# Performance work log

Measured on AMD Instinct MI355X. Metric: run time of the kernel, lower is better.

The kernel has to match this reference:

```python
import jax, jax.numpy as jnp
import numpy as np

N_USERS = 100000
N_ITEMS = 50000
DIM = 64
HID = 64
E = 3200000
B = 16384


def setup_inputs() -> dict:
    key = jax.random.key(0)
    ks = jax.random.split(key, 16)
    N = N_USERS + N_ITEMS
    return {
        "users": jax.random.randint(ks[0], (B,), 0, N_USERS),
        "items": jax.random.randint(ks[1], (B,), 0, N_ITEMS),
        "edge_index": jax.random.randint(ks[2], (2, E), 0, N),
        "edge_weight": jax.random.uniform(ks[3], (E,), dtype=jnp.float32),
        # learned parameters
        "U": jax.random.normal(ks[4], (N_USERS, DIM), jnp.float32) * 0.1,
        "I": jax.random.normal(ks[5], (N_ITEMS, DIM), jnp.float32) * 0.1,
        "W0": jax.random.normal(ks[6], (DIM, HID), jnp.float32) / np.sqrt(DIM),
        "b0": jnp.zeros((HID,), jnp.float32),
        "g0": jnp.ones((HID,), jnp.float32),
        "be0": jnp.zeros((HID,), jnp.float32),
        "W1": jax.random.normal(ks[7], (HID, HID), jnp.float32) / np.sqrt(HID),
        "b1": jnp.zeros((HID,), jnp.float32),
        "g1": jnp.ones((HID,), jnp.float32),
        "be1": jnp.zeros((HID,), jnp.float32),
        "Wp": jax.random.normal(ks[8], (HID, DIM), jnp.float32) / np.sqrt(HID),
        "bp": jnp.zeros((DIM,), jnp.float32),
        "bu": jnp.zeros((N_USERS,), jnp.float32),
        "bi": jnp.zeros((N_ITEMS,), jnp.float32),
        "mu": jnp.zeros((), jnp.float32),
    }


def _layernorm(h, g, b, eps=1e-5):
    m = jnp.mean(h, axis=-1, keepdims=True)
    v = jnp.mean(jnp.square(h - m), axis=-1, keepdims=True)
    return (h - m) * jax.lax.rsqrt(v + eps) * g + b


def reference(users, items, edge_index, edge_weight, U, I,
              W0, b0, g0, be0, W1, b1, g1, be1, Wp, bp, bu, bi, mu):
    N = U.shape[0] + I.shape[0]
    x = jnp.concatenate([U, I], axis=0)  # [N, DIM]

    # GCN normalization with added self-loops (torch_geometric gcn_norm)
    loop = jnp.arange(N)
    src = jnp.concatenate([edge_index[0], loop])
    dst = jnp.concatenate([edge_index[1], loop])
    ew = jnp.concatenate([edge_weight, jnp.ones((N,), edge_weight.dtype)])
    deg = jax.ops.segment_sum(ew, dst, num_segments=N)
    dinv = jnp.where(deg > 0, jax.lax.rsqrt(deg), 0.0)
    norm = dinv[src] * ew * dinv[dst]  # [E+N]

    def conv(h, W, b):
        hw = h @ W  # [N, HID]
        msgs = norm[:, None] * hw[src]  # gather: [E+N, HID]
        return jax.ops.segment_sum(msgs, dst, num_segments=N) + b

    # layer 0: conv -> layernorm -> relu -> (dropout=identity, eval) -> residual
    h = x
    h_in = h
    h = conv(h, W0, b0)
    h = jax.nn.relu(_layernorm(h, g0, be0)) + h_in
    # layer 1
    h_in = h
    h = conv(h, W1, b1)
    h = jax.nn.relu(_layernorm(h, g1, be1)) + h_in

    h = h @ Wp + bp  # proj_out: [N, DIM]
    h_user = h[:U.shape[0]]
    h_item = h[U.shape[0]:]

    s = jnp.sum(h_user[users] * h_item[items], axis=-1)
    s = s + bu[users] + bi[items] + mu
    return jnp.clip(s, 1.0, 5.0)
```

## Files before the change

kernel.cpp:

```cpp
#include <hip/hip_runtime.h>

#define NU 100000
#define NI 50000
#define NN 150000
#define D  64
#define CAP 47
#define OVF_MAX 4096

#define BINSHIFT 8
#define BINW 256
#define NBINS 586
#define BINCAP 5848
#define STAGE_CAP 12
#define EPT 4
#define SPILL_CAP 262144

typedef unsigned int uint;
typedef unsigned short ushort;

__device__ __forceinline__ float half_reduce_add(float v) {
    #pragma unroll
    for (int m = 16; m >= 1; m >>= 1) v += __shfl_xor(v, m, 64);
    return v;
}
__device__ __forceinline__ ushort f2bf(float f) {
    union { float f; uint i; } c; c.f = f;
    uint r = c.i + 0x7FFF + ((c.i >> 16) & 1);
    return (ushort)(r >> 16);
}
__device__ __forceinline__ float lane_bcast(float v, int l) {
    return __int_as_float(__builtin_amdgcn_readlane(__float_as_int(v), l));
}
__device__ __forceinline__ uint enc14(float w) {
    uint b = __float_as_uint(w) + 0x00020000u;
    return b & 0xFFFC0000u;
}
__device__ __forceinline__ float dec14(uint r) {
    return __uint_as_float(r & 0xFFFC0000u);
}
__device__ __forceinline__ void spill_one(int d, uint s, float w,
        uint2* __restrict__ spill, int* __restrict__ spillcnt) {
    int si = atomicAdd(spillcnt, 1);
    if (si < SPILL_CAP) spill[si] = make_uint2(s | enc14(w), (uint)d);
}

__global__ __launch_bounds__(256) void k_bin(
        const int* __restrict__ src, const int* __restrict__ dst,
        const float* __restrict__ ew, int* __restrict__ bincur,
        uint2* __restrict__ binbuf, uint2* __restrict__ spill,
        int* __restrict__ spillcnt, int E) {
    __shared__ uint2 stage[NBINS][STAGE_CAP];
    __shared__ int scnt[NBINS];
    int t = threadIdx.x;
    for (int i = t; i < NBINS; i += 256) scnt[i] = 0;
    __syncthreads();
    const int batch = 256 * EPT;
    for (int base = blockIdx.x * batch; base < E; base += gridDim.x * batch) {
        int dd[EPT]; uint ss[EPT]; float ww[EPT]; int ok[EPT];
        #pragma unroll
        for (int k = 0; k < EPT; ++k) {
            int e = base + k * 256 + t;
            ok[k] = (e < E);
            if (ok[k]) { dd[k] = dst[e]; ss[k] = (uint)src[e]; ww[k] = ew[e]; }
        }
        #pragma unroll
        for (int k = 0; k < EPT; ++k) {
            if (!ok[k]) continue;
            int bin = dd[k] >> BINSHIFT;
            int slot = atomicAdd(&scnt[bin], 1);
            if (slot < STAGE_CAP) {
                stage[bin][slot] = make_uint2(
                    ss[k] | ((uint)(dd[k] & (BINW - 1)) << 18),
                    (uint)__float_as_int(ww[k]));
            } else {
                spill_one(dd[k], ss[k], ww[k], spill, spillcnt);
            }
        }
        __syncthreads();
        for (int bin = t; bin < NBINS; bin += 256) {
            int c = scnt[bin]; if (c > STAGE_CAP) c = STAGE_CAP;
            while (c >= 8) {
                int b0 = atomicAdd(&bincur[bin], 8);
                if (b0 + 8 <= BINCAP) {
                    uint4* o4 = (uint4*)(binbuf + (size_t)bin * BINCAP + b0);
                    uint2* s2 = &stage[bin][c - 8];
                    o4[0] = make_uint4(s2[0].x, s2[0].y, s2[1].x, s2[1].y);
                    o4[1] = make_uint4(s2[2].x, s2[2].y, s2[3].x, s2[3].y);
                    o4[2] = make_uint4(s2[4].x, s2[4].y, s2[5].x, s2[5].y);
                    o4[3] = make_uint4(s2[6].x, s2[6].y, s2[7].x, s2[7].y);
                } else {
                    for (int j = 0; j < 8; ++j) {
                        uint2 r = stage[bin][c - 8 + j];
                        spill_one((bin << BINSHIFT) + (int)(r.x >> 18),
                                  r.x & 0x3FFFFu, __int_as_float((int)r.y),
                                  spill, spillcnt);
                    }
                }
                c -= 8;
            }
            scnt[bin] = c;
        }
        __syncthreads();
    }
    for (int bin = t; bin < NBINS; bin += 256) {
        int c = scnt[bin]; if (c > STAGE_CAP) c = STAGE_CAP;
        if (c > 0) {
            int b0 = atomicAdd(&bincur[bin], c);
            for (int j = 0; j < c; ++j) {
                uint2 r = stage[bin][j];
                if (b0 + j < BINCAP) binbuf[(size_t)bin * BINCAP + b0 + j] = r;
                else spill_one((bin << BINSHIFT) + (int)(r.x >> 18),
                               r.x & 0x3FFFFu, __int_as_float((int)r.y),
                               spill, spillcnt);
            }
        }
    }
}

__global__ __launch_bounds__(256) void k_regroup(
        const int* __restrict__ bincur, const uint2* __restrict__ binbuf,
        const uint2* __restrict__ spill, const int* __restrict__ spillcnt,
        uint* __restrict__ recs, int* __restrict__ cursor,
        float* __restrict__ dinv, int4* __restrict__ ovf,
        int* __restrict__ ovfcnt) {
    __shared__ uint image[256 * CAP];
    __shared__ int cnt[256];
    __shared__ float ovfw[256];
    int t = threadIdx.x;
    int bin = blockIdx.x;
    cnt[t] = 0; ovfw[t] = 0.0f;
    __syncthreads();
    int dbase = bin << BINSHIFT;
    int nrec = bincur[bin]; if (nrec > BINCAP) nrec = BINCAP;
    const uint2* bb = binbuf + (size_t)bin * BINCAP;
    for (int i = t; i < nrec; i += 256) {
        uint2 r = bb[i];
        int dl = (int)(r.x >> 18);
        int slot = atomicAdd(&cnt[dl], 1);
        uint s = r.x & 0x3FFFFu;
        float w = __int_as_float((int)r.y);
        if (slot < CAP) image[dl * CAP + slot] = enc14(w) | s;
        else {
            atomicAdd(&ovfw[dl], w);
            int o = atomicAdd(ovfcnt, 1);
            if (o < OVF_MAX)
                ovf[o] = make_int4(dbase + dl, (int)s, __float_as_int(w), 0);
        }
    }
    int ns = spillcnt[0]; if (ns > SPILL_CAP) ns = SPILL_CAP;
    for (int i = t; i < ns; i += 256) {
        uint2 e = spill[i];
        int d = (int)e.y;
        if (d < dbase || d >= dbase + BINW) continue;
        int dl = d - dbase;
        int slot = atomicAdd(&cnt[dl], 1);
        if (slot < CAP) image[dl * CAP + slot] = e.x;
        else {
            float w = dec14(e.x);
            atomicAdd(&ovfw[dl], w);
            int o = atomicAdd(ovfcnt, 1);
            if (o < OVF_MAX) ovf[o] = make_int4(d, (int)(e.x & 0x3FFFFu),
                                                __float_as_int(w), 0);
        }
    }
    __syncthreads();
    int ndl = NN - dbase; if (ndl > 256) ndl = 256;
    if (ndl <= 0) return;
    if (t < ndl) {
        int c = cnt[t];
        cursor[dbase + t] = c;
        if (c > CAP) c = CAP;
        float dg = ovfw[t];
        for (int j = 0; j < c; ++j) dg += dec14(image[t * CAP + j]);
        dinv[dbase + t] = rsqrtf(dg + 1.0f);
    }
    int tot = ndl * CAP;
    uint* out = recs + (size_t)dbase * CAP;
    for (int i = t; i < tot; i += 256) out[i] = image[i];
}

__global__ __launch_bounds__(256) void k_gemm(
        const float* __restrict__ h, const float* __restrict__ U,
        const float* __restrict__ I, const float* __restrict__ W,
        const float* __restrict__ dinv, ushort* __restrict__ out) {
    int lane = threadIdx.x & 63;
    float wreg[64];
    #pragma unroll
    for (int k = 0; k < 64; ++k) wreg[k] = W[k * 64 + lane];
    int wpb = blockDim.x >> 6;
    int wid = blockIdx.x * wpb + (threadIdx.x >> 6);
    int tw = gridDim.x * wpb;
    for (int n = wid; n < NN; n += tw) {
        float xv;
        if (h) xv = h[(size_t)n * D + lane];
        else   xv = (n < NU) ? U[(size_t)n * D + lane]
                             : I[(size_t)(n - NU) * D + lane];
        float acc = 0.f;
        #pragma unroll
        for (int k = 0; k < 64; ++k)
            acc = fmaf(lane_bcast(xv, k), wreg[k], acc);
        out[(size_t)n * D + lane] = f2bf(acc * dinv[n]);
    }
}

__device__ __forceinline__ float2 conv_accum2(int n, int lane,
        const uint* __restrict__ hw2p, const int* __restrict__ cursor,
        const uint* __restrict__ recs, const int4* __restrict__ ovf,
        const int* __restrict__ ovfcnt) {
    int cnt = __builtin_amdgcn_readfirstlane(cursor[n]);
    if (cnt > CAP) cnt = CAP;
    uint rv = (lane < cnt) ? recs[(size_t)n * CAP + lane] : 0u;
    int odd = lane >> 5;
    int laneoff = lane & 31;
    float ax = 0.f, ay = 0.f;
    int cp = (cnt + 7) & ~7;
    for (int j0 = 0; j0 < cp; j0 += 8) {
        #pragma unroll
        for (int k = 0; k < 4; ++k) {
            uint re = (uint)__builtin_amdgcn_readlane((int)rv, j0 + 2 * k);
            uint ro = (uint)__builtin_amdgcn_readlane((int)rv, j0 + 2 * k + 1);
            uint r  = odd ? ro : re;
            int   s = (int)(r & 0x3FFFFu);
            float w = dec14(r);
            uint x = hw2p[(size_t)s * 32 + laneoff];
            ax = fmaf(w, __int_as_float((int)(x << 16)), ax);
            ay = fmaf(w, __int_as_float((int)(x & 0xFFFF0000u)), ay);
        }
    }
    ax += __shfl_xor(ax, 32, 64);
    ay += __shfl_xor(ay, 32, 64);
    uint xs = hw2p[(size_t)n * 32 + laneoff];
    ax += __int_as_float((int)(xs << 16));
    ay += __int_as_float((int)(xs & 0xFFFF0000u));
    int novf = __builtin_amdgcn_readfirstlane(ovfcnt[0]);
    if (novf > 0) {
        if (novf > OVF_MAX) novf = OVF_MAX;
        for (int j = 0; j < novf; ++j) {
            int4 e = ovf[j];
            if (e.x == n) {
                float w = __int_as_float(e.z);
                uint x = hw2p[(size_t)e.y * 32 + laneoff];
                ax = fmaf(w, __int_as_float((int)(x << 16)), ax);
                ay = fmaf(w, __int_as_float((int)(x & 0xFFFF0000u)), ay);
            }
        }
    }
    return make_float2(ax, ay);
}

__device__ __forceinline__ float2 ln_relu2(float2 a, float di, int p,
        const float* __restrict__ b, const float* __restrict__ g,
        const float* __restrict__ be) {
    float2 bb = ((const float2*)b)[p];
    float v0 = fmaf(a.x, di, bb.x);
    float v1 = fmaf(a.y, di, bb.y);
    float m = half_reduce_add(v0 + v1) * (1.0f / 64.0f);
    float d0 = v0 - m, d1 = v1 - m;
    float var = half_reduce_add(d0 * d0 + d1 * d1) * (1.0f / 64.0f);
    float rs = rsqrtf(var + 1e-5f);
    float2 gg = ((const float2*)g)[p];
    float2 ee = ((const float2*)be)[p];
    return make_float2(fmaxf(fmaf(d0 * rs, gg.x, ee.x), 0.0f),
                       fmaxf(fmaf(d1 * rs, gg.y, ee.y), 0.0f));
}

__global__ __launch_bounds__(256) void k_conv1(
        const uint* __restrict__ hw2p, const int* __restrict__ cursor,
        const uint* __restrict__ recs, const int4* __restrict__ ovf,
        const int* __restrict__ ovfcnt, const float* __restrict__ dinv,
        const float* __restrict__ b, const float* __restrict__ g,
        const float* __restrict__ be, const float* __restrict__ U,
        const float* __restrict__ I, float* __restrict__ out) {
    int lane = threadIdx.x & 63;
    int n = __builtin_amdgcn_readfirstlane(blockIdx.x * 4 + (threadIdx.x >> 6));
    if (n >= NN) return;
    float2 a = conv_accum2(n, lane, hw2p, cursor, recs, ovf, ovfcnt);
    int p = lane & 31;
    float2 y = ln_relu2(a, dinv[n], p, b, g, be);
    const float* R = (n < NU) ? (U + (size_t)n * D) : (I + (size_t)(n - NU) * D);
    float2 rr = ((const float2*)R)[p];
    if (lane < 32)
        ((float2*)out)[(size_t)n * 32 + p] = make_float2(y.x + rr.x, y.y + rr.y);
}

__global__ __launch_bounds__(256) void k_conv2score(
        const uint* __restrict__ hw2p, const int* __restrict__ cursor,
        const uint* __restrict__ recs, const int4* __restrict__ ovf,
        const int* __restrict__ ovfcnt, const float* __restrict__ dinv,
        const float* __restrict__ b, const float* __restrict__ g,
        const float* __restrict__ be, const int* __restrict__ users,
        const int* __restrict__ items, const float* __restrict__ h1,
        const float* __restrict__ Wp, const float* __restrict__ bp,
        const float* __restrict__ bu, const float* __restrict__ bi,
        const float* __restrict__ mu, float* __restrict__ out, int B) {
    int lane = threadIdx.x & 63;
    float wreg[64];
    #pragma unroll
    for (int k = 0; k < 64; ++k) wreg[k] = Wp[k * 64 + lane];
    float bpl = bp[lane];
    int q = lane & 31;
    int wpb = blockDim.x >> 6;
    int wid = blockIdx.x * wpb + (threadIdx.x >> 6);
    int tw = gridDim.x * wpb;
    for (int p = wid; p < B; p += tw) {
        int un = users[p];
        int in = NU + items[p];
        int nu = __builtin_amdgcn_readfirstlane(un);
        float2 au = conv_accum2(nu, lane, hw2p, cursor, recs, ovf, ovfcnt);
        float2 yu = ln_relu2(au, dinv[nu], q, b, g, be);
        float2 ru = ((const float2*)h1)[(size_t)nu * 32 + q];
        float2 hu = make_float2(yu.x + ru.x, yu.y + ru.y);
        int ni = __builtin_amdgcn_readfirstlane(in);
        float2 ai = conv_accum2(ni, lane, hw2p, cursor, recs, ovf, ovfcnt);
        float2 yi = ln_relu2(ai, dinv[ni], q, b, g, be);
        float2 ri = ((const float2*)h1)[(size_t)ni * 32 + q];
        float2 hi = make_float2(yi.x + ri.x, yi.y + ri.y);
        float pu = bpl, pi = bpl;
        #pragma unroll
        for (int j = 0; j < 32; ++j) {
            pu = fmaf(lane_bcast(hu.x, j), wreg[2 * j], pu);
            pu = fmaf(lane_bcast(hu.y, j), wreg[2 * j + 1], pu);
            pi = fmaf(lane_bcast(hi.x, j), wreg[2 * j], pi);
            pi = fmaf(lane_bcast(hi.y, j), wreg[2 * j + 1], pi);
        }
        float t = pu * pi;
        #pragma unroll
        for (int m = 32; m >= 1; m >>= 1) t += __shfl_xor(t, m, 64);
        if (lane == 0) {
            t += bu[un] + bi[in - NU] + mu[0];
            out[p] = fminf(fmaxf(t, 1.0f), 5.0f);
        }
    }
}

extern "C" void kernel_launch(void* const* d_in, const int* in_sizes, int n_in,
                              void* d_out, int out_size, void* d_ws, size_t ws_size,
                              hipStream_t stream) {
    const int*   users = (const int*)d_in[0];
    const int*   items = (const int*)d_in[1];
    const int*   ei2   = (const int*)d_in[2];
    const float* ew    = (const float*)d_in[3];
    const float* U     = (const float*)d_in[4];
    const float* I     = (const float*)d_in[5];
    const float* W0    = (const float*)d_in[6];
    const float* b0    = (const float*)d_in[7];
    const float* g0    = (const float*)d_in[8];
    const float* be0   = (const float*)d_in[9];
    const float* W1    = (const float*)d_in[10];
    const float* b1    = (const float*)d_in[11];
    const float* g1    = (const float*)d_in[12];
    const float* be1   = (const float*)d_in[13];
    const float* Wp    = (const float*)d_in[14];
    const float* bp    = (const float*)d_in[15];
    const float* bu    = (const float*)d_in[16];
    const float* bi    = (const float*)d_in[17];
    const float* mu    = (const float*)d_in[18];

    int B = in_sizes[0];
    int E = in_sizes[2] / 2;
    const int* srcp = ei2;
    const int* dstp = ei2 + E;

    char* p = (char*)d_ws;
    auto alloc = [&](size_t bytes) -> char* {
        char* r = p;
        p += (bytes + 255) & ~(size_t)255;
        return r;
    };
    int*    cbuf    = (int*)  alloc((size_t)(NBINS + 8) * 4);
    int*    bincur  = cbuf;
    int*    spillcnt= cbuf + NBINS;
    int*    ovfcnt  = cbuf + NBINS + 1;
    int*    cursor  = (int*)  alloc((size_t)NN * 4);
    float*  dinv    = (float*)alloc((size_t)NN * 4);
    int4*   ovf     = (int4*) alloc((size_t)OVF_MAX * 16);
    uint2*  spill   = (uint2*)alloc((size_t)SPILL_CAP * 8);
    uint2*  binbuf  = (uint2*)alloc((size_t)NBINS * BINCAP * 8);
    uint*   recs    = (uint*) alloc((size_t)NN * CAP * 4);
    ushort* hw2b    = (ushort*)alloc((size_t)NN * D * 2);
    float*  h1      = (float*)alloc((size_t)NN * D * 4);
    const uint* hw2p = (const uint*)hw2b;

    hipMemsetAsync(cbuf, 0, (size_t)(NBINS + 8) * 4, stream);

    int gW = (NN + 3) / 4;

    k_bin<<<768, 256, 0, stream>>>(srcp, dstp, ew, bincur, binbuf,
                                   spill, spillcnt, E);
    k_regroup<<<NBINS, 256, 0, stream>>>(bincur, binbuf, spill, spillcnt,
                                         recs, cursor, dinv, ovf, ovfcnt);

    k_gemm<<<2048, 256, 0, stream>>>(nullptr, U, I, W0, dinv, hw2b);
    k_conv1<<<gW, 256, 0, stream>>>(hw2p, cursor, recs, ovf, ovfcnt, dinv,
                                    b0, g0, be0, U, I, h1);
    k_gemm<<<2048, 256, 0, stream>>>(h1, U, I, W1, dinv, hw2b);
    k_conv2score<<<1024, 256, 0, stream>>>(hw2p, cursor, recs, ovf, ovfcnt, dinv,
                                           b1, g1, be1, users, items, h1,
                                           Wp, bp, bu, bi, mu,
                                           (float*)d_out, B);
}
```

Measured before the change: 413.5 us.

## Fuse first GEMM into binning kernel, store h1 in bf16, pipeline conv gathers

The first GEMM now runs inside the binning launch on extra blocks so both overlap, and the dinv scaling is applied afterwards in the regroup kernel on the bf16 output. The layer-1 output h1 is stored as bf16 instead of fp32, which halves its write and read traffic in the second GEMM and the scoring kernel, at some cost in accuracy. The conv gather loop is rewritten as a software-pipelined, manually unrolled sequence using ds_bpermute with three register groups, so more gathers are in flight at once. The GEMM inner loops use four accumulators. Taken together these add rounding steps and register pressure.

```diff
diff --git a/kernel.cpp b/kernel.cpp
--- a/kernel.cpp
+++ b/kernel.cpp
@@ -14,6 +14,8 @@
 #define STAGE_CAP 12
 #define EPT 4
 #define SPILL_CAP 262144
+#define BIN_BLOCKS 768
+#define GEMM_BLOCKS 2048
 
 typedef unsigned int uint;
 typedef unsigned short ushort;
@@ -44,18 +46,42 @@
     if (si < SPILL_CAP) spill[si] = make_uint2(s | enc14(w), (uint)d);
 }
 
-__global__ __launch_bounds__(256) void k_bin(
+__global__ __launch_bounds__(256) void k_bin_gemm(
         const int* __restrict__ src, const int* __restrict__ dst,
         const float* __restrict__ ew, int* __restrict__ bincur,
         uint2* __restrict__ binbuf, uint2* __restrict__ spill,
-        int* __restrict__ spillcnt, int E) {
+        int* __restrict__ spillcnt, int E,
+        const float* __restrict__ U, const float* __restrict__ I,
+        const float* __restrict__ W0, ushort* __restrict__ hw2b) {
     __shared__ uint2 stage[NBINS][STAGE_CAP];
     __shared__ int scnt[NBINS];
+    if (blockIdx.x >= BIN_BLOCKS) {
+        int lane = threadIdx.x & 63;
+        float wreg[64];
+        #pragma unroll
+        for (int k = 0; k < 64; ++k) wreg[k] = W0[k * 64 + lane];
+        int wid = (blockIdx.x - BIN_BLOCKS) * 4 + (threadIdx.x >> 6);
+        int tw = GEMM_BLOCKS * 4;
+        for (int n = wid; n < NN; n += tw) {
+            float xv = (n < NU) ? U[(size_t)n * D + lane]
+                                : I[(size_t)(n - NU) * D + lane];
+            float a0 = 0.f, a1 = 0.f, a2 = 0.f, a3 = 0.f;
+            #pragma unroll
+            for (int k = 0; k < 64; k += 4) {
+                a0 = fmaf(lane_bcast(xv, k + 0), wreg[k + 0], a0);
+                a1 = fmaf(lane_bcast(xv, k + 1), wreg[k + 1], a1);
+                a2 = fmaf(lane_bcast(xv, k + 2), wreg[k + 2], a2);
+                a3 = fmaf(lane_bcast(xv, k + 3), wreg[k + 3], a3);
+            }
+            hw2b[(size_t)n * D + lane] = f2bf((a0 + a1) + (a2 + a3));
+        }
+        return;
+    }
     int t = threadIdx.x;
     for (int i = t; i < NBINS; i += 256) scnt[i] = 0;
     __syncthreads();
     const int batch = 256 * EPT;
-    for (int base = blockIdx.x * batch; base < E; base += gridDim.x * batch) {
+    for (int base = blockIdx.x * batch; base < E; base += BIN_BLOCKS * batch) {
         int dd[EPT]; uint ss[EPT]; float ww[EPT]; int ok[EPT];
         #pragma unroll
         for (int k = 0; k < EPT; ++k) {
@@ -122,7 +148,7 @@
         const uint2* __restrict__ spill, const int* __restrict__ spillcnt,
         uint* __restrict__ recs, int* __restrict__ cursor,
         float* __restrict__ dinv, int4* __restrict__ ovf,
-        int* __restrict__ ovfcnt) {
+        int* __restrict__ ovfcnt, ushort* __restrict__ hw2b) {
     __shared__ uint image[256 * CAP];
     __shared__ int cnt[256];
     __shared__ float ovfw[256];
@@ -172,34 +198,22 @@
         if (c > CAP) c = CAP;
         float dg = ovfw[t];
         for (int j = 0; j < c; ++j) dg += dec14(image[t * CAP + j]);
-        dinv[dbase + t] = rsqrtf(dg + 1.0f);
+        float dv = rsqrtf(dg + 1.0f);
+        dinv[dbase + t] = dv;
+        ovfw[t] = dv;
     }
     int tot = ndl * CAP;
     uint* out = recs + (size_t)dbase * CAP;
     for (int i = t; i < tot; i += 256) out[i] = image[i];
-}
-
-__global__ __launch_bounds__(256) void k_gemm(
-        const float* __restrict__ h, const float* __restrict__ U,
-        const float* __restrict__ I, const float* __restrict__ W,
-        const float* __restrict__ dinv, ushort* __restrict__ out) {
-    int lane = threadIdx.x & 63;
-    float wreg[64];
-    #pragma unroll
-    for (int k = 0; k < 64; ++k) wreg[k] = W[k * 64 + lane];
-    int wpb = blockDim.x >> 6;
-    int wid = blockIdx.x * wpb + (threadIdx.x >> 6);
-    int tw = gridDim.x * wpb;
-    for (int n = wid; n < NN; n += tw) {
-        float xv;
-        if (h) xv = h[(size_t)n * D + lane];
-        else   xv = (n < NU) ? U[(size_t)n * D + lane]
-                             : I[(size_t)(n - NU) * D + lane];
-        float acc = 0.f;
-        #pragma unroll
-        for (int k = 0; k < 64; ++k)
-            acc = fmaf(lane_bcast(xv, k), wreg[k], acc);
-        out[(size_t)n * D + lane] = f2bf(acc * dinv[n]);
+    __syncthreads();
+    uint* hw = (uint*)hw2b + (size_t)dbase * 32;
+    int tot32 = ndl * 32;
+    for (int i = t; i < tot32; i += 256) {
+        float di = ovfw[i >> 5];
+        uint v = hw[i];
+        uint lo = (uint)f2bf(__uint_as_float(v << 16) * di);
+        uint hi = (uint)f2bf(__uint_as_float(v & 0xFFFF0000u) * di);
+        hw[i] = lo | (hi << 16);
     }
 }
 
@@ -210,28 +224,50 @@
     int cnt = __builtin_amdgcn_readfirstlane(cursor[n]);
     if (cnt > CAP) cnt = CAP;
     uint rv = (lane < cnt) ? recs[(size_t)n * CAP + lane] : 0u;
-    int odd = lane >> 5;
-    int laneoff = lane & 31;
+    const int  vodd4 = (lane >> 5) << 2;
+    const uint lb4   = (uint)(lane & 31) << 2;
+    uint xs = *(const uint*)((const char*)hw2p + (((uint)n << 7) + lb4));
     float ax = 0.f, ay = 0.f;
     int cp = (cnt + 7) & ~7;
-    for (int j0 = 0; j0 < cp; j0 += 8) {
-        #pragma unroll
-        for (int k = 0; k < 4; ++k) {
-            uint re = (uint)__builtin_amdgcn_readlane((int)rv, j0 + 2 * k);
-            uint ro = (uint)__builtin_amdgcn_readlane((int)rv, j0 + 2 * k + 1);
-            uint r  = odd ? ro : re;
-            int   s = (int)(r & 0x3FFFFu);
-            float w = dec14(r);
-            uint x = hw2p[(size_t)s * 32 + laneoff];
-            ax = fmaf(w, __int_as_float((int)(x << 16)), ax);
-            ay = fmaf(w, __int_as_float((int)(x & 0xFFFF0000u)), ay);
-        }
-    }
+
+#define CA_DECL(c) uint x##c##0, x##c##1, x##c##2, x##c##3, \
+                        w##c##0, w##c##1, w##c##2, w##c##3;
+#define CA_GET(c, i, P) { \
+    uint r = (uint)__builtin_amdgcn_ds_bpermute(vodd4 + 8 * (P), (int)rv); \
+    w##c##i = r & 0xFFFC0000u; \
+    x##c##i = *(const uint*)((const char*)hw2p + \
+                             (((r & 0x3FFFFu) << 7) + lb4)); }
+#define CA_ISSUE(c, P0) { CA_GET(c, 0, (P0)+0) CA_GET(c, 1, (P0)+1) \
+                          CA_GET(c, 2, (P0)+2) CA_GET(c, 3, (P0)+3) }
+#define CA_FMA1(c, i) { \
+    ax = fmaf(__uint_as_float(w##c##i), __uint_as_float(x##c##i << 16), ax); \
+    ay = fmaf(__uint_as_float(w##c##i), \
+              __uint_as_float(x##c##i & 0xFFFF0000u), ay); }
+#define CA_FMA(c) { CA_FMA1(c,0) CA_FMA1(c,1) CA_FMA1(c,2) CA_FMA1(c,3) }
+
+    CA_DECL(A) CA_DECL(B) CA_DECL(G)
+    if (cp > 0)  CA_ISSUE(A, 0)
+    if (cp > 8)  CA_ISSUE(B, 4)
+    if (cp > 16) CA_ISSUE(G, 8)
+    if (cp > 0)  CA_FMA(A)
+    if (cp > 24) CA_ISSUE(A, 12)
+    if (cp > 8)  CA_FMA(B)
+    if (cp > 32) CA_ISSUE(B, 16)
+    if (cp > 16) CA_FMA(G)
+    if (cp > 40) CA_ISSUE(G, 20)
+    if (cp > 24) CA_FMA(A)
+    if (cp > 32) CA_FMA(B)
+    if (cp > 40) CA_FMA(G)
+#undef CA_FMA
+#undef CA_FMA1
+#undef CA_ISSUE
+#undef CA_GET
+#undef CA_DECL
+
     ax += __shfl_xor(ax, 32, 64);
     ay += __shfl_xor(ay, 32, 64);
-    uint xs = hw2p[(size_t)n * 32 + laneoff];
-    ax += __int_as_float((int)(xs << 16));
-    ay += __int_as_float((int)(xs & 0xFFFF0000u));
+    ax += __uint_as_float(xs << 16);
+    ay += __uint_as_float(xs & 0xFFFF0000u);
     int novf = __builtin_amdgcn_readfirstlane(ovfcnt[0]);
     if (novf > 0) {
         if (novf > OVF_MAX) novf = OVF_MAX;
@@ -239,7 +275,7 @@
             int4 e = ovf[j];
             if (e.x == n) {
                 float w = __int_as_float(e.z);
-                uint x = hw2p[(size_t)e.y * 32 + laneoff];
+                uint x = hw2p[(size_t)e.y * 32 + (lane & 31)];
                 ax = fmaf(w, __int_as_float((int)(x << 16)), ax);
                 ay = fmaf(w, __int_as_float((int)(x & 0xFFFF0000u)), ay);
             }
@@ -270,7 +306,7 @@
         const int* __restrict__ ovfcnt, const float* __restrict__ dinv,
         const float* __restrict__ b, const float* __restrict__ g,
         const float* __restrict__ be, const float* __restrict__ U,
-        const float* __restrict__ I, float* __restrict__ out) {
+        const float* __restrict__ I, uint* __restrict__ out1) {
     int lane = threadIdx.x & 63;
     int n = __builtin_amdgcn_readfirstlane(blockIdx.x * 4 + (threadIdx.x >> 6));
     if (n >= NN) return;
@@ -279,8 +315,34 @@
     float2 y = ln_relu2(a, dinv[n], p, b, g, be);
     const float* R = (n < NU) ? (U + (size_t)n * D) : (I + (size_t)(n - NU) * D);
     float2 rr = ((const float2*)R)[p];
-    if (lane < 32)
-        ((float2*)out)[(size_t)n * 32 + p] = make_float2(y.x + rr.x, y.y + rr.y);
+    if (lane < 32) {
+        out1[(size_t)n * 32 + p] =
+            (uint)f2bf(y.x + rr.x) | ((uint)f2bf(y.y + rr.y) << 16);
+    }
+}
+
+__global__ __launch_bounds__(256) void k_gemm2(
+        const ushort* __restrict__ hb, const float* __restrict__ W,
+        const float* __restrict__ dinv, ushort* __restrict__ out) {
+    int lane = threadIdx.x & 63;
+    float wreg[64];
+    #pragma unroll
+    for (int k = 0; k < 64; ++k) wreg[k] = W[k * 64 + lane];
+    int wpb = blockDim.x >> 6;
+    int wid = blockIdx.x * wpb + (threadIdx.x >> 6);
+    int tw = gridDim.x * wpb;
+    for (int n = wid; n < NN; n += tw) {
+        float xv = __uint_as_float((uint)hb[(size_t)n * D + lane] << 16);
+        float a0 = 0.f, a1 = 0.f, a2 = 0.f, a3 = 0.f;
+        #pragma unroll
+        for (int k = 0; k < 64; k += 4) {
+            a0 = fmaf(lane_bcast(xv, k + 0), wreg[k + 0], a0);
+            a1 = fmaf(lane_bcast(xv, k + 1), wreg[k + 1], a1);
+            a2 = fmaf(lane_bcast(xv, k + 2), wreg[k + 2], a2);
+            a3 = fmaf(lane_bcast(xv, k + 3), wreg[k + 3], a3);
+        }
+        out[(size_t)n * D + lane] = f2bf(((a0 + a1) + (a2 + a3)) * dinv[n]);
+    }
 }
 
 __global__ __launch_bounds__(256) void k_conv2score(
@@ -289,7 +351,7 @@
         const int* __restrict__ ovfcnt, const float* __restrict__ dinv,
         const float* __restrict__ b, const float* __restrict__ g,
         const float* __restrict__ be, const int* __restrict__ users,
-        const int* __restrict__ items, const float* __restrict__ h1,
+        const int* __restrict__ items, const uint* __restrict__ h1b,
         const float* __restrict__ Wp, const float* __restrict__ bp,
         const float* __restrict__ bu, const float* __restrict__ bi,
         const float* __restrict__ mu, float* __restrict__ out, int B) {
@@ -308,13 +370,15 @@
         int nu = __builtin_amdgcn_readfirstlane(un);
         float2 au = conv_accum2(nu, lane, hw2p, cursor, recs, ovf, ovfcnt);
         float2 yu = ln_relu2(au, dinv[nu], q, b, g, be);
-        float2 ru = ((const float2*)h1)[(size_t)nu * 32 + q];
-        float2 hu = make_float2(yu.x + ru.x, yu.y + ru.y);
+        uint xu = h1b[(size_t)nu * 32 + q];
+        float2 hu = make_float2(yu.x + __uint_as_float(xu << 16),
+                                yu.y + __uint_as_float(xu & 0xFFFF0000u));
         int ni = __builtin_amdgcn_readfirstlane(in);
         float2 ai = conv_accum2(ni, lane, hw2p, cursor, recs, ovf, ovfcnt);
         float2 yi = ln_relu2(ai, dinv[ni], q, b, g, be);
-        float2 ri = ((const float2*)h1)[(size_t)ni * 32 + q];
-        float2 hi = make_float2(yi.x + ri.x, yi.y + ri.y);
+        uint xi = h1b[(size_t)ni * 32 + q];
+        float2 hi = make_float2(yi.x + __uint_as_float(xi << 16),
+                                yi.y + __uint_as_float(xi & 0xFFFF0000u));
         float pu = bpl, pi = bpl;
         #pragma unroll
         for (int j = 0; j < 32; ++j) {
@@ -378,24 +442,23 @@
     uint2*  binbuf  = (uint2*)alloc((size_t)NBINS * BINCAP * 8);
     uint*   recs    = (uint*) alloc((size_t)NN * CAP * 4);
     ushort* hw2b    = (ushort*)alloc((size_t)NN * D * 2);
-    float*  h1      = (float*)alloc((size_t)NN * D * 4);
+    uint*   h1b     = (uint*) alloc((size_t)NN * 32 * 4);
     const uint* hw2p = (const uint*)hw2b;
 
     hipMemsetAsync(cbuf, 0, (size_t)(NBINS + 8) * 4, stream);
 
     int gW = (NN + 3) / 4;
 
-    k_bin<<<768, 256, 0, stream>>>(srcp, dstp, ew, bincur, binbuf,
-                                   spill, spillcnt, E);
+    k_bin_gemm<<<BIN_BLOCKS + GEMM_BLOCKS, 256, 0, stream>>>(
+        srcp, dstp, ew, bincur, binbuf, spill, spillcnt, E, U, I, W0, hw2b);
     k_regroup<<<NBINS, 256, 0, stream>>>(bincur, binbuf, spill, spillcnt,
-                                         recs, cursor, dinv, ovf, ovfcnt);
-
-    k_gemm<<<2048, 256, 0, stream>>>(nullptr, U, I, W0, dinv, hw2b);
+                                         recs, cursor, dinv, ovf, ovfcnt, hw2b);
+
     k_conv1<<<gW, 256, 0, stream>>>(hw2p, cursor, recs, ovf, ovfcnt, dinv,
-                                    b0, g0, be0, U, I, h1);
-    k_gemm<<<2048, 256, 0, stream>>>(h1, U, I, W1, dinv, hw2b);
+                                    b0, g0, be0, U, I, h1b);
+    k_gemm2<<<2048, 256, 0, stream>>>((const ushort*)h1b, W1, dinv, hw2b);
     k_conv2score<<<1024, 256, 0, stream>>>(hw2p, cursor, recs, ovf, ovfcnt, dinv,
-                                           b1, g1, be1, users, items, h1,
+                                           b1, g1, be1, users, items, h1b,
                                            Wp, bp, bu, bi, mu,
                                            (float*)d_out, B);
 }
```

After: 430.8 us. +4.2%, slower.
